# Kernel optimization log

Measured on AMD Instinct MI355X. Metric: run time of the kernel, lower is better.

## Reference

```python
import jax, jax.numpy as jnp
import numpy as np

N = 100000      # nodes
E = 1600000     # edges (avg degree 16)
F_IN = 128      # num_features
H = 64          # num_hidden
C = 40          # num_classes


def setup_inputs() -> dict:
    key = jax.random.key(0)
    ks = jax.random.split(key, 12)
    glorot = lambda k, fi, fo: jax.random.normal(k, (fi, fo), jnp.float32) * np.float32(1.0 / np.sqrt(fi))
    return {
        "x": jax.random.normal(ks[0], (N, F_IN), jnp.float32),
        "edge_index": jax.random.randint(ks[1], (2, E), 0, N, jnp.int64),
        "conv0_w": glorot(ks[2], F_IN, H), "conv0_b": jnp.zeros((H,), jnp.float32),
        "lin0_w": glorot(ks[3], H, H),     "lin0_b": jnp.zeros((H,), jnp.float32),
        "conv1_w": glorot(ks[4], H, H),    "conv1_b": jnp.zeros((H,), jnp.float32),
        "lin1_w": glorot(ks[5], H, H),     "lin1_b": jnp.zeros((H,), jnp.float32),
        "out_w": glorot(ks[6], 2 * H, C),  "out_b": jnp.zeros((C,), jnp.float32),
    }


def _gcn_conv(h, W, b, src, dst, norm, n):
    # h: [N, din] -> transform then symmetric-normalized scatter-add aggregation
    m = (h @ W)[src] * norm[:, None]           # [E+N, dout] gathered messages
    return jax.ops.segment_sum(m, dst, num_segments=n) + b


def reference(x, edge_index, conv0_w, conv0_b, lin0_w, lin0_b,
              conv1_w, conv1_b, lin1_w, lin1_b, out_w, out_b):
    n = x.shape[0]
    loops = jnp.arange(n, dtype=edge_index.dtype)
    src = jnp.concatenate([edge_index[0], loops])  # self-loops appended (GCNConv default)
    dst = jnp.concatenate([edge_index[1], loops])
    deg = jax.ops.segment_sum(jnp.ones_like(dst, x.dtype), dst, num_segments=n)
    dinv = jnp.where(deg > 0, jax.lax.rsqrt(deg), 0.0)
    norm = dinv[src] * dinv[dst]                   # D^-1/2 A D^-1/2 edge weights

    # layer 0 (dropout omitted: eval mode for deterministic reference)
    h = jax.nn.elu(_gcn_conv(x, conv0_w, conv0_b, src, dst, norm, n))
    y0 = h @ lin0_w + lin0_b
    # layer 1
    h = jax.nn.elu(_gcn_conv(h, conv1_w, conv1_b, src, dst, norm, n))
    y1 = h @ lin1_w + lin1_b

    z = jnp.concatenate([y0, y1], axis=1)          # [N, 2H] jumping-knowledge concat
    return z @ out_w + out_b                       # [N, C]
```

## Files before the change

### kernel.cpp

```cpp
#include <hip/hip_runtime.h>

#define DEVFN __device__ __forceinline__

typedef __attribute__((ext_vector_type(8))) short short8;
typedef __attribute__((ext_vector_type(4))) float float4v;

DEVFN float bf2f(unsigned short u) {
    union { unsigned int i; float f; } c;
    c.i = ((unsigned int)u) << 16;
    return c.f;
}

DEVFN unsigned short f2bf(float f) {
    union { float f; unsigned int i; } c;
    c.f = f;
    unsigned int u = c.i;
    return (unsigned short)((u + 0x7FFFu + ((u >> 16) & 1u)) >> 16);
}

DEVFN void addu4(float* acc, uint4 u) {
    unsigned int w[4] = {u.x, u.y, u.z, u.w};
#pragma unroll
    for (int k = 0; k < 4; k++) {
        union { unsigned int i; float f; } lo, hi;
        lo.i = w[k] << 16;
        hi.i = w[k] & 0xFFFF0000u;
        acc[2 * k]     += lo.f;
        acc[2 * k + 1] += hi.f;
    }
}

#define CHUNK 4096

__global__ __launch_bounds__(256) void k_scat(const int* __restrict__ src,
                                              const int* __restrict__ dst,
                                              int* __restrict__ gcnt,
                                              unsigned int* __restrict__ part,
                                              int E, int STRIDE) {
    __shared__ int lh[1024];
    __shared__ int lb[1024];
    int t = threadIdx.x;
    for (int b = t; b < 1024; b += 256) lh[b] = 0;
    __syncthreads();
    int i0 = blockIdx.x * CHUNK;
    int d[16];
#pragma unroll
    for (int k = 0; k < 16; k++) {
        int idx = i0 + k * 256 + t;
        d[k] = (idx < E) ? dst[idx] : -1;
        if (d[k] >= 0) atomicAdd(&lh[d[k] >> 8], 1);
    }
    __syncthreads();
    for (int b = t; b < 1024; b += 256) {
        int c = lh[b];
        if (c > 0) lb[b] = b * STRIDE + atomicAdd(&gcnt[b], c);
        lh[b] = 0;
    }
    __syncthreads();
#pragma unroll
    for (int k = 0; k < 16; k++) {
        if (d[k] >= 0) {
            int idx = i0 + k * 256 + t;
            int s = src[idx];
            int b = d[k] >> 8;
            int r = atomicAdd(&lh[b], 1);
            part[lb[b] + r] = (unsigned int)s | ((unsigned int)(d[k] & 255) << 24);
        }
    }
}

__global__ __launch_bounds__(256) void k_fill2(const unsigned int* __restrict__ part,
                                               const int* __restrict__ gcnt,
                                               float* __restrict__ dinv,
                                               int* __restrict__ roff,
                                               int* __restrict__ csr, int n, int STRIDE) {
    __shared__ int lcnt[256];
    __shared__ int lsc[256];
    __shared__ int lcur[256];
    int b = blockIdx.x, t = threadIdx.x;
    int cnt = gcnt[b];
    int s0 = b * STRIDE;
    lcnt[t] = 0;
    __syncthreads();
    for (int i = t; i < cnt; i += 256) atomicAdd(&lcnt[part[s0 + i] >> 24], 1);
    __syncthreads();
    int v = lcnt[t];
    lsc[t] = v;
    __syncthreads();
    for (int o = 1; o < 256; o <<= 1) {
        int x = (t >= o) ? lsc[t - o] : 0;
        __syncthreads();
        lsc[t] += x;
        __syncthreads();
    }
    int excl = lsc[t] - v;
    int node = (b << 8) + t;
    if (node < n) {
        dinv[node] = rsqrtf((float)(v + 1));
        roff[node] = s0 + excl + v;
    }
    lcur[t] = s0 + excl;
    __syncthreads();
    for (int i = t; i < cnt; i += 256) {
        unsigned int p = part[s0 + i];
        int pos = atomicAdd(&lcur[p >> 24], 1);
        csr[pos] = (int)(p & 0xFFFFFFu);
    }
}

__global__ __launch_bounds__(256) void k_prep(const float* __restrict__ W0,
                                              const float* __restrict__ W1,
                                              const float* __restrict__ lin0_w, const float* __restrict__ lin0_b,
                                              const float* __restrict__ lin1_w, const float* __restrict__ lin1_b,
                                              const float* __restrict__ out_w, const float* __restrict__ out_b,
                                              unsigned short* __restrict__ Wb0,
                                              unsigned short* __restrict__ Wb1,
                                              unsigned short* __restrict__ Wfb0,
                                              unsigned short* __restrict__ Wfb1,
                                              float* __restrict__ bfv,
                                              unsigned short* __restrict__ Ab,
                                              unsigned short* __restrict__ Ab2, int n) {
    int tid = blockIdx.x * 256 + threadIdx.x;
    if (tid < 1024) {
        int ks = tid >> 8, rem = tid & 255;
        int nt = rem >> 6, lane = rem & 63;
        int quad = lane >> 4, c = lane & 15;
        union { unsigned short h[8]; uint4 u; } p;
#pragma unroll
        for (int j = 0; j < 8; j++)
            p.h[j] = f2bf(W0[(ks * 32 + quad * 8 + j) * 64 + nt * 16 + c]);
        *(uint4*)(Wb0 + (size_t)tid * 8) = p.u;
    } else if (tid < 1536) {
        int t2 = tid - 1024;
        int ks = t2 >> 8, rem = t2 & 255;
        int nt = rem >> 6, lane = rem & 63;
        int quad = lane >> 4, c = lane & 15;
        union { unsigned short h[8]; uint4 u; } p;
#pragma unroll
        for (int j = 0; j < 8; j++)
            p.h[j] = f2bf(W1[(ks * 32 + quad * 8 + j) * 64 + nt * 16 + c]);
        *(uint4*)(Wb1 + (size_t)t2 * 8) = p.u;
    } else if (tid < 1920) {
        int t2 = tid - 1536;
        int ks = t2 / 192;
        int rem = t2 % 192;
        int nt = rem >> 6, lane = rem & 63;
        int quad = lane >> 4, c = lane & 15;
        int col = nt * 16 + c;
        union { unsigned short h[8]; uint4 u; } p;
#pragma unroll
        for (int j = 0; j < 8; j++) {
            unsigned short r = 0;
            if (col < 40) {
                int i = ks * 32 + quad * 8 + j;
                float a = 0.f;
                for (int k = 0; k < 64; k++) a += lin0_w[i * 64 + k] * out_w[k * 40 + col];
                r = f2bf(a);
            }
            p.h[j] = r;
        }
        *(uint4*)(Wfb0 + ((size_t)(ks * 3 + nt) * 64 + lane) * 8) = p.u;
    } else if (tid < 2304) {
        int t2 = tid - 1920;
        int ks = t2 / 192;
        int rem = t2 % 192;
        int nt = rem >> 6, lane = rem & 63;
        int quad = lane >> 4, c = lane & 15;
        int col = nt * 16 + c;
        union { unsigned short h[8]; uint4 u; } p;
#pragma unroll
        for (int j = 0; j < 8; j++) {
            unsigned short r = 0;
            if (col < 40) {
                int i = ks * 32 + quad * 8 + j;
                float a = 0.f;
                for (int k = 0; k < 64; k++) a += lin1_w[i * 64 + k] * out_w[(64 + k) * 40 + col];
                r = f2bf(a);
            }
            p.h[j] = r;
        }
        *(uint4*)(Wfb1 + ((size_t)(ks * 3 + nt) * 64 + lane) * 8) = p.u;
    } else if (tid < 2344) {
        int j = tid - 2304;
        float a = out_b[j];
        for (int k = 0; k < 64; k++) {
            a += lin0_b[k] * out_w[k * 40 + j];
            a += lin1_b[k] * out_w[(64 + k) * 40 + j];
        }
        bfv[j] = a;
    } else if (tid < 2352) {
        uint4 z = {0u, 0u, 0u, 0u};
        *(uint4*)(Ab + (size_t)n * 64 + (tid - 2344) * 8) = z;
    } else if (tid < 2360) {
        uint4 z = {0u, 0u, 0u, 0u};
        *(uint4*)(Ab2 + (size_t)n * 64 + (tid - 2352) * 8) = z;
    }
}


__global__ __launch_bounds__(256) void k_gemm_128(const float* __restrict__ A,
                                                  const unsigned short* __restrict__ Wb,
                                                  const float* __restrict__ dinv,
                                                  unsigned short* __restrict__ Cb, int n) {
    __shared__ unsigned short aLDS[64 * 144];
    int t = threadIdx.x;
    int r0 = blockIdx.x * 64;
    for (int idx = t; idx < 2048; idx += 256) {
        int r = idx >> 5;
        int k = (idx & 31) << 2;
        int gr = r0 + r; if (gr >= n) gr = n - 1;
        float4 u = *(const float4*)(A + (size_t)gr * 128 + k);
        int tile = r >> 4, m = r & 15;
        int ks = k >> 5, quad = (k >> 3) & 3, j0 = k & 7;
        int g = (tile * 4 + ks) * 4 + quad;
        union { unsigned short h[4]; uint2 u2; } pk;
        pk.h[0] = f2bf(u.x); pk.h[1] = f2bf(u.y); pk.h[2] = f2bf(u.z); pk.h[3] = f2bf(u.w);
        *(uint2*)(aLDS + g * 144 + m * 8 + j0) = pk.u2;
    }
    int lane = t & 63;
    int w = t >> 6;
    short8 bfr[4][4];
#pragma unroll
    for (int ks = 0; ks < 4; ks++)
#pragma unroll
        for (int nt = 0; nt < 4; nt++)
            bfr[ks][nt] = *(const short8*)(Wb + ((size_t)(ks * 4 + nt) * 64 + lane) * 8);
    __syncthreads();
    int quad = lane >> 4, m = lane & 15;
    short8 afr[4];
#pragma unroll
    for (int ks = 0; ks < 4; ks++)
        afr[ks] = *(const short8*)(aLDS + ((w * 4 + ks) * 4 + quad) * 144 + m * 8);
    float4v acc[4] = {};
#pragma unroll
    for (int nt = 0; nt < 4; nt++)
#pragma unroll
        for (int ks = 0; ks < 4; ks++)
            acc[nt] = __builtin_amdgcn_mfma_f32_16x16x32_bf16(afr[ks], bfr[ks][nt], acc[nt], 0, 0, 0);
    float dv[4];
#pragma unroll
    for (int reg = 0; reg < 4; reg++) {
        int gr = r0 + w * 16 + quad * 4 + reg;
        dv[reg] = (gr < n) ? dinv[gr] : 0.f;
    }
#pragma unroll
    for (int nt = 0; nt < 4; nt++)
#pragma unroll
        for (int reg = 0; reg < 4; reg++) {
            int gr = r0 + w * 16 + quad * 4 + reg;
            if (gr < n) Cb[(size_t)gr * 64 + nt * 16 + m] = f2bf(dv[reg] * acc[nt][reg]);
        }
}

DEVFN void agg_loop(const unsigned short* __restrict__ T, const int* __restrict__ csr,
                    int start, int end, int hb, int sub, int q, int h, float* acc) {
    for (int base = start; base < end; base += 32) {
        int m = end - base; if (m > 32) m = 32;
        int e = (sub < m) ? csr[base + sub] : 0;
        int j = 0;
        for (; j + 16 <= m; j += 16) {
            int s0 = __shfl(e, hb + j + q);
            int s1 = __shfl(e, hb + j + 4 + q);
            int s2 = __shfl(e, hb + j + 8 + q);
            int s3 = __shfl(e, hb + j + 12 + q);
            uint4 u0 = *(const uint4*)(T + (size_t)s0 * 64 + h * 8);
            uint4 u1 = *(const uint4*)(T + (size_t)s1 * 64 + h * 8);
            uint4 u2 = *(const uint4*)(T + (size_t)s2 * 64 + h * 8);
            uint4 u3 = *(const uint4*)(T + (size_t)s3 * 64 + h * 8);
            addu4(acc, u0); addu4(acc, u1); addu4(acc, u2); addu4(acc, u3);
        }
        if (j + 8 <= m) {
            int s0 = __shfl(e, hb + j + q);
            int s1 = __shfl(e, hb + j + 4 + q);
            uint4 u0 = *(const uint4*)(T + (size_t)s0 * 64 + h * 8);
            uint4 u1 = *(const uint4*)(T + (size_t)s1 * 64 + h * 8);
            addu4(acc, u0); addu4(acc, u1);
            j += 8;
        }
        if (j + 4 <= m) {
            int s = __shfl(e, hb + j + q);
            uint4 u = *(const uint4*)(T + (size_t)s * 64 + h * 8);
            addu4(acc, u);
            j += 4;
        }
        if (j < m) {
            int jj = j + q;
            int s = __shfl(e, hb + (jj & 31));
            if (jj < m) {
                uint4 u = *(const uint4*)(T + (size_t)s * 64 + h * 8);
                addu4(acc, u);
            }
        }
    }
}

DEVFN void gather2(const unsigned short* __restrict__ T, const int* __restrict__ csr,
                   const int* __restrict__ roffE, int v0, int n, int stride,
                   int hb, int sub, int q, int h,
                   float* accA, float* accB, float& dvA, float& dvB) {
    int v1 = v0 + 1;
    bool has1 = (v1 < n);
    int sA = ((v0 & 255) == 0) ? (v0 >> 8) * stride : roffE[v0 - 1];
    int eA = roffE[v0];
    int eB = has1 ? roffE[v1] : eA;
    int mA = eA - sA;
    int mB = eB - eA;
    dvA = rsqrtf((float)(mA + 1));
    dvB = rsqrtf((float)(mB + 1));
    uint4 uSA = {0u, 0u, 0u, 0u}, uSB = {0u, 0u, 0u, 0u};
    if (q == 0) {
        uSA = *(const uint4*)(T + (size_t)v0 * 64 + h * 8);
        if (has1) uSB = *(const uint4*)(T + (size_t)v1 * 64 + h * 8);
    }
    if (mA <= 32 && mB <= 32) {
        int e0 = (sub < mA) ? csr[sA + sub] : n;
        int e1 = (sub < mB) ? csr[eA + sub] : n;
        int a0 = __shfl(e0, hb + q),      a1 = __shfl(e0, hb + 4 + q);
        int a2 = __shfl(e0, hb + 8 + q),  a3 = __shfl(e0, hb + 12 + q);
        int b0 = __shfl(e1, hb + q),      b1 = __shfl(e1, hb + 4 + q);
        int b2 = __shfl(e1, hb + 8 + q),  b3 = __shfl(e1, hb + 12 + q);
        uint4 uA0 = *(const uint4*)(T + (size_t)a0 * 64 + h * 8);
        uint4 uA1 = *(const uint4*)(T + (size_t)a1 * 64 + h * 8);
        uint4 uA2 = *(const uint4*)(T + (size_t)a2 * 64 + h * 8);
        uint4 uA3 = *(const uint4*)(T + (size_t)a3 * 64 + h * 8);
        uint4 uB0 = *(const uint4*)(T + (size_t)b0 * 64 + h * 8);
        uint4 uB1 = *(const uint4*)(T + (size_t)b1 * 64 + h * 8);
        uint4 uB2 = *(const uint4*)(T + (size_t)b2 * 64 + h * 8);
        uint4 uB3 = *(const uint4*)(T + (size_t)b3 * 64 + h * 8);
        bool tA = (mA > 16), tB = (mB > 16);
        if (tA) {
            int a4 = __shfl(e0, hb + 16 + q), a5 = __shfl(e0, hb + 20 + q);
            int a6 = __shfl(e0, hb + 24 + q), a7 = __shfl(e0, hb + 28 + q);
            uint4 u4 = *(const uint4*)(T + (size_t)a4 * 64 + h * 8);
            uint4 u5 = *(const uint4*)(T + (size_t)a5 * 64 + h * 8);
            uint4 u6 = *(const uint4*)(T + (size_t)a6 * 64 + h * 8);
            uint4 u7 = *(const uint4*)(T + (size_t)a7 * 64 + h * 8);
            addu4(accA, u4); addu4(accA, u5); addu4(accA, u6); addu4(accA, u7);
        }
        if (tB) {
            int b4 = __shfl(e1, hb + 16 + q), b5 = __shfl(e1, hb + 20 + q);
            int b6 = __shfl(e1, hb + 24 + q), b7 = __shfl(e1, hb + 28 + q);
            uint4 u4 = *(const uint4*)(T + (size_t)b4 * 64 + h * 8);
            uint4 u5 = *(const uint4*)(T + (size_t)b5 * 64 + h * 8);
            uint4 u6 = *(const uint4*)(T + (size_t)b6 * 64 + h * 8);
            uint4 u7 = *(const uint4*)(T + (size_t)b7 * 64 + h * 8);
            addu4(accB, u4); addu4(accB, u5); addu4(accB, u6); addu4(accB, u7);
        }
        addu4(accA, uA0); addu4(accA, uA1); addu4(accA, uA2); addu4(accA, uA3);
        addu4(accB, uB0); addu4(accB, uB1); addu4(accB, uB2); addu4(accB, uB3);
    } else {
        agg_loop(T, csr, sA, eA, hb, sub, q, h, accA);
        agg_loop(T, csr, eA, eB, hb, sub, q, h, accB);
    }
    addu4(accA, uSA);
    addu4(accB, uSB);
}

__global__ __launch_bounds__(256) void k_aggmid(const unsigned short* __restrict__ T,
                                                const int* __restrict__ csr,
                                                const int* __restrict__ roffE,
                                                const float* __restrict__ bias,
                                                const unsigned short* __restrict__ WbG,
                                                const unsigned short* __restrict__ WbH,
                                                const float* __restrict__ dinv,
                                                unsigned short* __restrict__ Ab2,
                                                float* __restrict__ O, int n, int stride) {
    __shared__ unsigned short aLDS[8 * 144];
    int t = threadIdx.x;
    int lane = t & 63, w = t >> 6;
    int half = lane >> 5, sub = lane & 31;
    int q = sub >> 3, h = sub & 7;
    int hb = half << 5;
    int lv = w * 4 + half * 2;
    int v0 = blockIdx.x * 16 + lv;
    bool act = (v0 < n);
    float accA[8] = {0.f, 0.f, 0.f, 0.f, 0.f, 0.f, 0.f, 0.f};
    float accB[8] = {0.f, 0.f, 0.f, 0.f, 0.f, 0.f, 0.f, 0.f};
    float dvA = 0.f, dvB = 0.f;
    if (act) gather2(T, csr, roffE, v0, n, stride, hb, sub, q, h, accA, accB, dvA, dvB);
#pragma unroll
    for (int i = 0; i < 8; i++) {
        accA[i] += __shfl_xor(accA[i], 8);
        accA[i] += __shfl_xor(accA[i], 16);
        accB[i] += __shfl_xor(accB[i], 8);
        accB[i] += __shfl_xor(accB[i], 16);
    }
    if (act && q == 0) {
        float4 b0 = *(const float4*)(bias + h * 8);
        float4 b1 = *(const float4*)(bias + h * 8 + 4);
        float bb[8] = {b0.x, b0.y, b0.z, b0.w, b1.x, b1.y, b1.z, b1.w};
        union { unsigned short hh[8]; uint4 u; } pA, pB;
#pragma unroll
        for (int i = 0; i < 8; i++) {
            float rA = dvA * accA[i] + bb[i];
            rA = (rA > 0.f) ? rA : (__expf(rA) - 1.f);
            pA.hh[i] = f2bf(rA);
            float rB = dvB * accB[i] + bb[i];
            rB = (rB > 0.f) ? rB : (__expf(rB) - 1.f);
            pB.hh[i] = f2bf(rB);
        }
        *(uint4*)(aLDS + h * 144 + lv * 8) = pA.u;
        if (v0 + 1 < n) *(uint4*)(aLDS + h * 144 + (lv + 1) * 8) = pB.u;
    }
    __syncthreads();
    int quad = lane >> 4, m = lane & 15;
    short8 afr[2];
#pragma unroll
    for (int ks = 0; ks < 2; ks++)
        afr[ks] = *(const short8*)(aLDS + (ks * 4 + quad) * 144 + m * 8);
    int r0 = blockIdx.x * 16;
    if (w < 2) {
        int nt0 = w * 2;
        float4v a0 = {}, a1 = {};
#pragma unroll
        for (int ks = 0; ks < 2; ks++) {
            short8 bf0 = *(const short8*)(WbG + ((size_t)(ks * 4 + nt0) * 64 + lane) * 8);
            short8 bf1 = *(const short8*)(WbG + ((size_t)(ks * 4 + nt0 + 1) * 64 + lane) * 8);
            a0 = __builtin_amdgcn_mfma_f32_16x16x32_bf16(afr[ks], bf0, a0, 0, 0, 0);
            a1 = __builtin_amdgcn_mfma_f32_16x16x32_bf16(afr[ks], bf1, a1, 0, 0, 0);
        }
#pragma unroll
        for (int reg = 0; reg < 4; reg++) {
            int gr = r0 + quad * 4 + reg;
            if (gr < n) {
                float dv = dinv[gr];
                Ab2[(size_t)gr * 64 + nt0 * 16 + m]       = f2bf(dv * a0[reg]);
                Ab2[(size_t)gr * 64 + (nt0 + 1) * 16 + m] = f2bf(dv * a1[reg]);
            }
        }
    } else {
        int nt0 = (w - 2) * 2;
        int ntc = (w == 2) ? 2 : 1;
        float4v a0 = {}, a1 = {};
#pragma unroll
        for (int ks = 0; ks < 2; ks++) {
            short8 bf0 = *(const short8*)(WbH + ((size_t)(ks * 3 + nt0) * 64 + lane) * 8);
            a0 = __builtin_amdgcn_mfma_f32_16x16x32_bf16(afr[ks], bf0, a0, 0, 0, 0);
        }
        if (ntc == 2) {
#pragma unroll
            for (int ks = 0; ks < 2; ks++) {
                short8 bf1 = *(const short8*)(WbH + ((size_t)(ks * 3 + nt0 + 1) * 64 + lane) * 8);
                a1 = __builtin_amdgcn_mfma_f32_16x16x32_bf16(afr[ks], bf1, a1, 0, 0, 0);
            }
        }
        int col0 = nt0 * 16 + m;
        if (col0 < 40) {
#pragma unroll
            for (int reg = 0; reg < 4; reg++) {
                int gr = r0 + quad * 4 + reg;
                if (gr < n) O[(size_t)gr * 40 + col0] = a0[reg];
            }
        }
        if (ntc == 2) {
            int col1 = (nt0 + 1) * 16 + m;
            if (col1 < 40) {
#pragma unroll
                for (int reg = 0; reg < 4; reg++) {
                    int gr = r0 + quad * 4 + reg;
                    if (gr < n) O[(size_t)gr * 40 + col1] = a1[reg];
                }
            }
        }
    }
}

__global__ __launch_bounds__(256) void k_agghead(const unsigned short* __restrict__ T,
                                                 const int* __restrict__ csr,
                                                 const int* __restrict__ roffE,
                                                 const float* __restrict__ bias,
                                                 const unsigned short* __restrict__ Wfb,
                                                 const float* __restrict__ bfv,
                                                 float* __restrict__ O, int n, int stride) {
    __shared__ unsigned short aLDS[8 * 144];
    int t = threadIdx.x;
    int lane = t & 63, w = t >> 6;
    int half = lane >> 5, sub = lane & 31;
    int q = sub >> 3, h = sub & 7;
    int hb = half << 5;
    int lv = w * 4 + half * 2;
    int v0 = blockIdx.x * 16 + lv;
    bool act = (v0 < n);
    float accA[8] = {0.f, 0.f, 0.f, 0.f, 0.f, 0.f, 0.f, 0.f};
    float accB[8] = {0.f, 0.f, 0.f, 0.f, 0.f, 0.f, 0.f, 0.f};
    float dvA = 0.f, dvB = 0.f;
    if (act) gather2(T, csr, roffE, v0, n, stride, hb, sub, q, h, accA, accB, dvA, dvB);
#pragma unroll
    for (int i = 0; i < 8; i++) {
        accA[i] += __shfl_xor(accA[i], 8);
        accA[i] += __shfl_xor(accA[i], 16);
        accB[i] += __shfl_xor(accB[i], 8);
        accB[i] += __shfl_xor(accB[i], 16);
    }
    if (act && q == 0) {
        float4 b0 = *(const float4*)(bias + h * 8);
        float4 b1 = *(const float4*)(bias + h * 8 + 4);
        float bb[8] = {b0.x, b0.y, b0.z, b0.w, b1.x, b1.y, b1.z, b1.w};
        union { unsigned short hh[8]; uint4 u; } pA, pB;
#pragma unroll
        for (int i = 0; i < 8; i++) {
            float rA = dvA * accA[i] + bb[i];
            rA = (rA > 0.f) ? rA : (__expf(rA) - 1.f);
            pA.hh[i] = f2bf(rA);
            float rB = dvB * accB[i] + bb[i];
            rB = (rB > 0.f) ? rB : (__expf(rB) - 1.f);
            pB.hh[i] = f2bf(rB);
        }
        *(uint4*)(aLDS + h * 144 + lv * 8) = pA.u;
        if (v0 + 1 < n) *(uint4*)(aLDS + h * 144 + (lv + 1) * 8) = pB.u;
    }
    __syncthreads();
    int quad = lane >> 4, m = lane & 15;
    short8 afr[2];
#pragma unroll
    for (int ks = 0; ks < 2; ks++)
        afr[ks] = *(const short8*)(aLDS + (ks * 4 + quad) * 144 + m * 8);
    int r0 = blockIdx.x * 16;
    if (w < 3) {
        float4v a0 = {};
#pragma unroll
        for (int ks = 0; ks < 2; ks++) {
            short8 bf0 = *(const short8*)(Wfb + ((size_t)(ks * 3 + w) * 64 + lane) * 8);
            a0 = __builtin_amdgcn_mfma_f32_16x16x32_bf16(afr[ks], bf0, a0, 0, 0, 0);
        }
        int col = w * 16 + m;
        if (col < 40) {
            float bb = bfv[col];
#pragma unroll
            for (int reg = 0; reg < 4; reg++) {
                int gr = r0 + quad * 4 + reg;
                if (gr < n) {
                    size_t p = (size_t)gr * 40 + col;
                    O[p] = O[p] + a0[reg] + bb;
                }
            }
        }
    }
}


extern "C" void kernel_launch(void* const* d_in, const int* in_sizes, int n_in,
                              void* d_out, int out_size, void* d_ws, size_t ws_size,
                              hipStream_t stream) {
    const float* x       = (const float*)d_in[0];
    const int*   eidx    = (const int*)d_in[1];
    const float* conv0_w = (const float*)d_in[2];
    const float* conv0_b = (const float*)d_in[3];
    const float* lin0_w  = (const float*)d_in[4];
    const float* lin0_b  = (const float*)d_in[5];
    const float* conv1_w = (const float*)d_in[6];
    const float* conv1_b = (const float*)d_in[7];
    const float* lin1_w  = (const float*)d_in[8];
    const float* lin1_b  = (const float*)d_in[9];
    const float* out_w   = (const float*)d_in[10];
    const float* out_b   = (const float*)d_in[11];

    int n = in_sizes[0] / 128;
    int E = in_sizes[1] / 2;
    const int* src = eidx;
    const int* dst = eidx + E;
    int NBUK = (n + 255) >> 8;
    int gC = (E + CHUNK - 1) / CHUNK;
    int STRIDE = ((E / NBUK) * 3 / 2 + 1024 + 255) & ~255;

    char* wsb = (char*)d_ws;
    auto al = [](size_t v) { return (v + 4095) & ~(size_t)4095; };
    size_t o = 0;
    int*            gcnt  = (int*)(wsb + o);            o = al(o + 1024 * 4);
    float*          dinv  = (float*)(wsb + o);          o = al(o + (size_t)n * 4);
    int*            roff  = (int*)(wsb + o);            o = al(o + (size_t)n * 4);
    unsigned int*   part  = (unsigned int*)(wsb + o);   o = al(o + (size_t)NBUK * STRIDE * 4);
    int*            csr   = (int*)(wsb + o);            o = al(o + (size_t)NBUK * STRIDE * 4);
    float*          bfv   = (float*)(wsb + o);          o = al(o + 40 * 4);
    unsigned short* Wb0   = (unsigned short*)(wsb + o); o = al(o + 8192 * 2);
    unsigned short* Wb1   = (unsigned short*)(wsb + o); o = al(o + 4096 * 2);
    unsigned short* Wfb0  = (unsigned short*)(wsb + o); o = al(o + 3072 * 2);
    unsigned short* Wfb1  = (unsigned short*)(wsb + o); o = al(o + 3072 * 2);
    unsigned short* Ab    = (unsigned short*)(wsb + o); o = al(o + (size_t)(n + 1) * 64 * 2);
    unsigned short* Ab2   = (unsigned short*)(wsb + o); o = al(o + (size_t)(n + 1) * 64 * 2);
    float* O = (float*)d_out;

    int gT = (n + 63) / 64;
    int gV2 = (n + 15) / 16;

    hipMemsetAsync(gcnt, 0, 1024 * 4, stream);
    k_scat<<<gC, 256, 0, stream>>>(src, dst, gcnt, part, E, STRIDE);
    k_fill2<<<NBUK, 256, 0, stream>>>(part, gcnt, dinv, roff, csr, n, STRIDE);
    k_prep<<<10, 256, 0, stream>>>(conv0_w, conv1_w, lin0_w, lin0_b, lin1_w, lin1_b,
                                   out_w, out_b, Wb0, Wb1, Wfb0, Wfb1, bfv, Ab, Ab2, n);

    k_gemm_128<<<gT, 256, 0, stream>>>(x, Wb0, dinv, Ab, n);
    k_aggmid<<<gV2, 256, 0, stream>>>(Ab, csr, roff, conv0_b, Wb1, Wfb0, dinv, Ab2, O, n, STRIDE);
    k_agghead<<<gV2, 256, 0, stream>>>(Ab2, csr, roff, conv1_b, Wfb1, bfv, O, n, STRIDE);
}
```

Baseline: 256.3 us.

## Defer layer-0 head projection to final kernel and cache buckets in LDS

The middle aggregation kernel no longer computes the layer-0 contribution to the 40-column output. It writes the post-ELU hidden h0 as bf16, and the head kernel reloads it and does both output GEMMs, writing O once instead of read-modify-write. k_fill2 keeps bucket entries in shared memory so the second pass skips re-reading global part. The aggregation accumulators become float2 vectors, aiming for packed adds. This trades an extra 128-byte-per-node write and read of h0 for dropping the fp32 40-wide O write, its read-back, and the MFMA work in the mid kernel.

```diff
diff --git a/kernel.cpp b/kernel.cpp
--- a/kernel.cpp
+++ b/kernel.cpp
@@ -4,6 +4,7 @@
 
 typedef __attribute__((ext_vector_type(8))) short short8;
 typedef __attribute__((ext_vector_type(4))) float float4v;
+typedef __attribute__((ext_vector_type(2))) float f32x2;
 
 DEVFN float bf2f(unsigned short u) {
     union { unsigned int i; float f; } c;
@@ -18,15 +19,17 @@
     return (unsigned short)((u + 0x7FFFu + ((u >> 16) & 1u)) >> 16);
 }
 
-DEVFN void addu4(float* acc, uint4 u) {
+DEVFN void addu4(f32x2* acc, uint4 u) {
     unsigned int w[4] = {u.x, u.y, u.z, u.w};
 #pragma unroll
     for (int k = 0; k < 4; k++) {
         union { unsigned int i; float f; } lo, hi;
         lo.i = w[k] << 16;
         hi.i = w[k] & 0xFFFF0000u;
-        acc[2 * k]     += lo.f;
-        acc[2 * k + 1] += hi.f;
+        f32x2 v;
+        v.x = lo.f;
+        v.y = hi.f;
+        acc[k] += v;
     }
 }
 
@@ -74,15 +77,25 @@
                                                float* __restrict__ dinv,
                                                int* __restrict__ roff,
                                                int* __restrict__ csr, int n, int STRIDE) {
+    __shared__ unsigned int ent[8192];
     __shared__ int lcnt[256];
     __shared__ int lsc[256];
     __shared__ int lcur[256];
     int b = blockIdx.x, t = threadIdx.x;
     int cnt = gcnt[b];
     int s0 = b * STRIDE;
+    bool fits = (cnt <= 8192);
     lcnt[t] = 0;
     __syncthreads();
-    for (int i = t; i < cnt; i += 256) atomicAdd(&lcnt[part[s0 + i] >> 24], 1);
+    if (fits) {
+        for (int i = t; i < cnt; i += 256) {
+            unsigned int p = part[s0 + i];
+            ent[i] = p;
+            atomicAdd(&lcnt[p >> 24], 1);
+        }
+    } else {
+        for (int i = t; i < cnt; i += 256) atomicAdd(&lcnt[part[s0 + i] >> 24], 1);
+    }
     __syncthreads();
     int v = lcnt[t];
     lsc[t] = v;
@@ -101,10 +114,18 @@
     }
     lcur[t] = s0 + excl;
     __syncthreads();
-    for (int i = t; i < cnt; i += 256) {
-        unsigned int p = part[s0 + i];
-        int pos = atomicAdd(&lcur[p >> 24], 1);
-        csr[pos] = (int)(p & 0xFFFFFFu);
+    if (fits) {
+        for (int i = t; i < cnt; i += 256) {
+            unsigned int p = ent[i];
+            int pos = atomicAdd(&lcur[p >> 24], 1);
+            csr[pos] = (int)(p & 0xFFFFFFu);
+        }
+    } else {
+        for (int i = t; i < cnt; i += 256) {
+            unsigned int p = part[s0 + i];
+            int pos = atomicAdd(&lcur[p >> 24], 1);
+            csr[pos] = (int)(p & 0xFFFFFFu);
+        }
     }
 }
 
@@ -253,7 +274,7 @@
 }
 
 DEVFN void agg_loop(const unsigned short* __restrict__ T, const int* __restrict__ csr,
-                    int start, int end, int hb, int sub, int q, int h, float* acc) {
+                    int start, int end, int hb, int sub, int q, int h, f32x2* acc) {
     for (int base = start; base < end; base += 32) {
         int m = end - base; if (m > 32) m = 32;
         int e = (sub < m) ? csr[base + sub] : 0;
@@ -297,7 +318,7 @@
 DEVFN void gather2(const unsigned short* __restrict__ T, const int* __restrict__ csr,
                    const int* __restrict__ roffE, int v0, int n, int stride,
                    int hb, int sub, int q, int h,
-                   float* accA, float* accB, float& dvA, float& dvB) {
+                   f32x2* accA, f32x2* accB, float& dvA, float& dvB) {
     int v1 = v0 + 1;
     bool has1 = (v1 < n);
     int sA = ((v0 & 255) == 0) ? (v0 >> 8) * stride : roffE[v0 - 1];
@@ -356,15 +377,25 @@
     addu4(accB, uSB);
 }
 
+DEVFN void qreduce(f32x2* acc) {
+#pragma unroll
+    for (int k = 0; k < 4; k++) {
+        acc[k].x += __shfl_xor(acc[k].x, 8);
+        acc[k].x += __shfl_xor(acc[k].x, 16);
+        acc[k].y += __shfl_xor(acc[k].y, 8);
+        acc[k].y += __shfl_xor(acc[k].y, 16);
+    }
+}
+
 __global__ __launch_bounds__(256) void k_aggmid(const unsigned short* __restrict__ T,
                                                 const int* __restrict__ csr,
                                                 const int* __restrict__ roffE,
                                                 const float* __restrict__ bias,
                                                 const unsigned short* __restrict__ WbG,
-                                                const unsigned short* __restrict__ WbH,
                                                 const float* __restrict__ dinv,
                                                 unsigned short* __restrict__ Ab2,
-                                                float* __restrict__ O, int n, int stride) {
+                                                unsigned short* __restrict__ H0b,
+                                                int n, int stride) {
     __shared__ unsigned short aLDS[8 * 144];
     int t = threadIdx.x;
     int lane = t & 63, w = t >> 6;
@@ -374,28 +405,25 @@
     int lv = w * 4 + half * 2;
     int v0 = blockIdx.x * 16 + lv;
     bool act = (v0 < n);
-    float accA[8] = {0.f, 0.f, 0.f, 0.f, 0.f, 0.f, 0.f, 0.f};
-    float accB[8] = {0.f, 0.f, 0.f, 0.f, 0.f, 0.f, 0.f, 0.f};
+    f32x2 accA[4] = {};
+    f32x2 accB[4] = {};
     float dvA = 0.f, dvB = 0.f;
     if (act) gather2(T, csr, roffE, v0, n, stride, hb, sub, q, h, accA, accB, dvA, dvB);
-#pragma unroll
-    for (int i = 0; i < 8; i++) {
-        accA[i] += __shfl_xor(accA[i], 8);
-        accA[i] += __shfl_xor(accA[i], 16);
-        accB[i] += __shfl_xor(accB[i], 8);
-        accB[i] += __shfl_xor(accB[i], 16);
-    }
+    qreduce(accA);
+    qreduce(accB);
     if (act && q == 0) {
         float4 b0 = *(const float4*)(bias + h * 8);
         float4 b1 = *(const float4*)(bias + h * 8 + 4);
         float bb[8] = {b0.x, b0.y, b0.z, b0.w, b1.x, b1.y, b1.z, b1.w};
+        float aA[8] = {accA[0].x, accA[0].y, accA[1].x, accA[1].y, accA[2].x, accA[2].y, accA[3].x, accA[3].y};
+        float aB[8] = {accB[0].x, accB[0].y, accB[1].x, accB[1].y, accB[2].x, accB[2].y, accB[3].x, accB[3].y};
         union { unsigned short hh[8]; uint4 u; } pA, pB;
 #pragma unroll
         for (int i = 0; i < 8; i++) {
-            float rA = dvA * accA[i] + bb[i];
+            float rA = dvA * aA[i] + bb[i];
             rA = (rA > 0.f) ? rA : (__expf(rA) - 1.f);
             pA.hh[i] = f2bf(rA);
-            float rB = dvB * accB[i] + bb[i];
+            float rB = dvB * aB[i] + bb[i];
             rB = (rB > 0.f) ? rB : (__expf(rB) - 1.f);
             pB.hh[i] = f2bf(rB);
         }
@@ -404,12 +432,12 @@
     }
     __syncthreads();
     int quad = lane >> 4, m = lane & 15;
-    short8 afr[2];
-#pragma unroll
-    for (int ks = 0; ks < 2; ks++)
-        afr[ks] = *(const short8*)(aLDS + (ks * 4 + quad) * 144 + m * 8);
     int r0 = blockIdx.x * 16;
     if (w < 2) {
+        short8 afr[2];
+#pragma unroll
+        for (int ks = 0; ks < 2; ks++)
+            afr[ks] = *(const short8*)(aLDS + (ks * 4 + quad) * 144 + m * 8);
         int nt0 = w * 2;
         float4v a0 = {}, a1 = {};
 #pragma unroll
@@ -429,38 +457,12 @@
             }
         }
     } else {
-        int nt0 = (w - 2) * 2;
-        int ntc = (w == 2) ? 2 : 1;
-        float4v a0 = {}, a1 = {};
-#pragma unroll
-        for (int ks = 0; ks < 2; ks++) {
-            short8 bf0 = *(const short8*)(WbH + ((size_t)(ks * 3 + nt0) * 64 + lane) * 8);
-            a0 = __builtin_amdgcn_mfma_f32_16x16x32_bf16(afr[ks], bf0, a0, 0, 0, 0);
-        }
-        if (ntc == 2) {
-#pragma unroll
-            for (int ks = 0; ks < 2; ks++) {
-                short8 bf1 = *(const short8*)(WbH + ((size_t)(ks * 3 + nt0 + 1) * 64 + lane) * 8);
-                a1 = __builtin_amdgcn_mfma_f32_16x16x32_bf16(afr[ks], bf1, a1, 0, 0, 0);
-            }
-        }
-        int col0 = nt0 * 16 + m;
-        if (col0 < 40) {
-#pragma unroll
-            for (int reg = 0; reg < 4; reg++) {
-                int gr = r0 + quad * 4 + reg;
-                if (gr < n) O[(size_t)gr * 40 + col0] = a0[reg];
-            }
-        }
-        if (ntc == 2) {
-            int col1 = (nt0 + 1) * 16 + m;
-            if (col1 < 40) {
-#pragma unroll
-                for (int reg = 0; reg < 4; reg++) {
-                    int gr = r0 + quad * 4 + reg;
-                    if (gr < n) O[(size_t)gr * 40 + col1] = a1[reg];
-                }
-            }
+        int t2 = t - 128;
+        int r = t2 >> 3, c = t2 & 7;
+        int gr = r0 + r;
+        if (gr < n) {
+            uint4 u = *(const uint4*)(aLDS + c * 144 + r * 8);
+            *(uint4*)(H0b + (size_t)gr * 64 + c * 8) = u;
         }
     }
 }
@@ -469,10 +471,13 @@
                                                  const int* __restrict__ csr,
                                                  const int* __restrict__ roffE,
                                                  const float* __restrict__ bias,
-                                                 const unsigned short* __restrict__ Wfb,
+                                                 const unsigned short* __restrict__ H0b,
+                                                 const unsigned short* __restrict__ Wfb0,
+                                                 const unsigned short* __restrict__ Wfb1,
                                                  const float* __restrict__ bfv,
                                                  float* __restrict__ O, int n, int stride) {
     __shared__ unsigned short aLDS[8 * 144];
+    __shared__ unsigned short aLDS0[8 * 144];
     int t = threadIdx.x;
     int lane = t & 63, w = t >> 6;
     int half = lane >> 5, sub = lane & 31;
@@ -481,28 +486,31 @@
     int lv = w * 4 + half * 2;
     int v0 = blockIdx.x * 16 + lv;
     bool act = (v0 < n);
-    float accA[8] = {0.f, 0.f, 0.f, 0.f, 0.f, 0.f, 0.f, 0.f};
-    float accB[8] = {0.f, 0.f, 0.f, 0.f, 0.f, 0.f, 0.f, 0.f};
+    if (t < 128) {
+        int r = t >> 3, c = t & 7;
+        int gr = blockIdx.x * 16 + r; if (gr >= n) gr = n - 1;
+        uint4 u = *(const uint4*)(H0b + (size_t)gr * 64 + c * 8);
+        *(uint4*)(aLDS0 + c * 144 + r * 8) = u;
+    }
+    f32x2 accA[4] = {};
+    f32x2 accB[4] = {};
     float dvA = 0.f, dvB = 0.f;
     if (act) gather2(T, csr, roffE, v0, n, stride, hb, sub, q, h, accA, accB, dvA, dvB);
-#pragma unroll
-    for (int i = 0; i < 8; i++) {
-        accA[i] += __shfl_xor(accA[i], 8);
-        accA[i] += __shfl_xor(accA[i], 16);
-        accB[i] += __shfl_xor(accB[i], 8);
-        accB[i] += __shfl_xor(accB[i], 16);
-    }
+    qreduce(accA);
+    qreduce(accB);
     if (act && q == 0) {
         float4 b0 = *(const float4*)(bias + h * 8);
         float4 b1 = *(const float4*)(bias + h * 8 + 4);
         float bb[8] = {b0.x, b0.y, b0.z, b0.w, b1.x, b1.y, b1.z, b1.w};
+        float aA[8] = {accA[0].x, accA[0].y, accA[1].x, accA[1].y, accA[2].x, accA[2].y, accA[3].x, accA[3].y};
+        float aB[8] = {accB[0].x, accB[0].y, accB[1].x, accB[1].y, accB[2].x, accB[2].y, accB[3].x, accB[3].y};
         union { unsigned short hh[8]; uint4 u; } pA, pB;
 #pragma unroll
         for (int i = 0; i < 8; i++) {
-            float rA = dvA * accA[i] + bb[i];
+            float rA = dvA * aA[i] + bb[i];
             rA = (rA > 0.f) ? rA : (__expf(rA) - 1.f);
             pA.hh[i] = f2bf(rA);
-            float rB = dvB * accB[i] + bb[i];
+            float rB = dvB * aB[i] + bb[i];
             rB = (rB > 0.f) ? rB : (__expf(rB) - 1.f);
             pB.hh[i] = f2bf(rB);
         }
@@ -511,17 +519,24 @@
     }
     __syncthreads();
     int quad = lane >> 4, m = lane & 15;
-    short8 afr[2];
-#pragma unroll
-    for (int ks = 0; ks < 2; ks++)
-        afr[ks] = *(const short8*)(aLDS + (ks * 4 + quad) * 144 + m * 8);
     int r0 = blockIdx.x * 16;
     if (w < 3) {
-        float4v a0 = {};
+        short8 h0fr[2], h1fr[2];
 #pragma unroll
         for (int ks = 0; ks < 2; ks++) {
-            short8 bf0 = *(const short8*)(Wfb + ((size_t)(ks * 3 + w) * 64 + lane) * 8);
-            a0 = __builtin_amdgcn_mfma_f32_16x16x32_bf16(afr[ks], bf0, a0, 0, 0, 0);
+            h0fr[ks] = *(const short8*)(aLDS0 + (ks * 4 + quad) * 144 + m * 8);
+            h1fr[ks] = *(const short8*)(aLDS  + (ks * 4 + quad) * 144 + m * 8);
+        }
+        float4v a0 = {}, a1 = {};
+#pragma unroll
+        for (int ks = 0; ks < 2; ks++) {
+            short8 bf0 = *(const short8*)(Wfb0 + ((size_t)(ks * 3 + w) * 64 + lane) * 8);
+            a0 = __builtin_amdgcn_mfma_f32_16x16x32_bf16(h0fr[ks], bf0, a0, 0, 0, 0);
+        }
+#pragma unroll
+        for (int ks = 0; ks < 2; ks++) {
+            short8 bf1 = *(const short8*)(Wfb1 + ((size_t)(ks * 3 + w) * 64 + lane) * 8);
+            a1 = __builtin_amdgcn_mfma_f32_16x16x32_bf16(h1fr[ks], bf1, a1, 0, 0, 0);
         }
         int col = w * 16 + m;
         if (col < 40) {
@@ -530,8 +545,7 @@
             for (int reg = 0; reg < 4; reg++) {
                 int gr = r0 + quad * 4 + reg;
                 if (gr < n) {
-                    size_t p = (size_t)gr * 40 + col;
-                    O[p] = O[p] + a0[reg] + bb;
+                    O[(size_t)gr * 40 + col] = a0[reg] + a1[reg] + bb;
                 }
             }
         }
@@ -578,6 +592,7 @@
     unsigned short* Wfb1  = (unsigned short*)(wsb + o); o = al(o + 3072 * 2);
     unsigned short* Ab    = (unsigned short*)(wsb + o); o = al(o + (size_t)(n + 1) * 64 * 2);
     unsigned short* Ab2   = (unsigned short*)(wsb + o); o = al(o + (size_t)(n + 1) * 64 * 2);
+    unsigned short* H0b   = (unsigned short*)(wsb + o); o = al(o + (size_t)n * 64 * 2);
     float* O = (float*)d_out;
 
     int gT = (n + 63) / 64;
@@ -590,6 +605,6 @@
                                    out_w, out_b, Wb0, Wb1, Wfb0, Wfb1, bfv, Ab, Ab2, n);
 
     k_gemm_128<<<gT, 256, 0, stream>>>(x, Wb0, dinv, Ab, n);
-    k_aggmid<<<gV2, 256, 0, stream>>>(Ab, csr, roff, conv0_b, Wb1, Wfb0, dinv, Ab2, O, n, STRIDE);
-    k_agghead<<<gV2, 256, 0, stream>>>(Ab2, csr, roff, conv1_b, Wfb1, bfv, O, n, STRIDE);
-}
+    k_aggmid<<<gV2, 256, 0, stream>>>(Ab, csr, roff, conv0_b, Wb1, dinv, Ab2, H0b, n, STRIDE);
+    k_agghead<<<gV2, 256, 0, stream>>>(Ab2, csr, roff, conv1_b, H0b, Wfb0, Wfb1, bfv, O, n, STRIDE);
+}
```

Measured after the change: 254.3 us. About the same (-0.8%).
